# Kernel tuning notes

Hardware: AMD Instinct MI355X
Metric: run time of the kernel (lower is better)

The kernel has to match this reference:

```python
import jax, jax.numpy as jnp
import numpy as np

D = 1024          # d_input_feature
GCN_OUTS = [1024, 512, 256]
DEC_OUTS = [512, 1024, 1024]  # reversed[1:] + [d_input_feature]
EPS = 1e-3        # keras LayerNormalization default epsilon


def _ln(x, gamma, beta):
    m = jnp.mean(x, axis=-1, keepdims=True)
    v = jnp.mean(jnp.square(x - m), axis=-1, keepdims=True)
    return gamma * (x - m) * jax.lax.rsqrt(v + EPS) + beta


def _gcn(x, A, W, b, act):
    # message passing with dense adjacency: act((A @ x) @ W + b)
    h = jnp.einsum('bij,bjd->bid', A, x)
    return act(h @ W + b)


def setup_inputs() -> dict:
    key = jax.random.key(0)
    ks = jax.random.split(key, 40)
    B, DG, DC, NTT = 16384, 772, 100, 128
    inp = {
        't_1': jax.random.randint(ks[0], (B,), 0, NTT),
        'g_1': jax.random.normal(ks[1], (B, DG), jnp.float32),
        'c_1': jax.random.normal(ks[2], (B, DC), jnp.float32),
        'A_1': jax.random.uniform(ks[3], (B, 3, 3), jnp.float32),
        't_2': jax.random.randint(ks[4], (B,), 0, NTT),
        'g_2': jax.random.normal(ks[5], (B, DG), jnp.float32),
        'c_2': jax.random.normal(ks[6], (B, DC), jnp.float32),
        'A_2': jax.random.uniform(ks[7], (B, 3, 3), jnp.float32),
        'embed': jax.random.normal(ks[8], (NTT, D), jnp.float32) * 0.02,
        'Wt': jax.random.normal(ks[9], (D, D), jnp.float32) / np.sqrt(D),
        'bt': jnp.zeros((D,), jnp.float32),
        'Wg': jax.random.normal(ks[10], (DG, D), jnp.float32) / np.sqrt(DG),
        'bg': jnp.zeros((D,), jnp.float32),
        'Wc': jax.random.normal(ks[11], (DC, D), jnp.float32) / np.sqrt(DC),
        'bc': jnp.zeros((D,), jnp.float32),
        'ln_t_g': jnp.ones((D,), jnp.float32), 'ln_t_b': jnp.zeros((D,), jnp.float32),
        'ln_g_g': jnp.ones((D,), jnp.float32), 'ln_g_b': jnp.zeros((D,), jnp.float32),
        'ln_c_g': jnp.ones((D,), jnp.float32), 'ln_c_b': jnp.zeros((D,), jnp.float32),
    }
    d_in = D
    for i, d_out in enumerate(GCN_OUTS):
        inp[f'enc_W{i}'] = jax.random.normal(ks[12 + i], (d_in, d_out), jnp.float32) / np.sqrt(d_in)
        inp[f'enc_b{i}'] = jnp.zeros((d_out,), jnp.float32)
        d_in = d_out
    for i, d_out in enumerate(DEC_OUTS):
        inp[f'dec_W{i}'] = jax.random.normal(ks[20 + i], (d_in, d_out), jnp.float32) / np.sqrt(d_in)
        inp[f'dec_b{i}'] = jnp.zeros((d_out,), jnp.float32)
        d_in = d_out
    return inp


def _branch(t, g, c, embed, Wt, bt, Wg, bg, Wc, bc,
            ln_t_g, ln_t_b, ln_g_g, ln_g_b, ln_c_g, ln_c_b):
    te = embed[t]                               # [B, D]
    te = jax.nn.relu(te @ Wt + bt)
    ge = jax.nn.relu(g @ Wg + bg)
    ce = jax.nn.relu(c @ Wc + bc)
    te = _ln(te, ln_t_g, ln_t_b)
    ge = _ln(ge, ln_g_g, ln_g_b)
    ce = _ln(ce, ln_c_g, ln_c_b)
    return jnp.stack([te, ge, ce], axis=1)      # [B, 3, D]


def _encoder(X, A, enc):
    x = X
    for W, b in enc:
        x = _gcn(x, A, W, b, jax.nn.relu)
    return x


def _decoder(Z, A, dec):
    x = Z
    for W, b in dec:
        x = _gcn(x, A, W, b, jax.nn.silu)       # swish
    return x


def reference(t_1, g_1, c_1, A_1, t_2, g_2, c_2, A_2,
              embed, Wt, bt, Wg, bg, Wc, bc,
              ln_t_g, ln_t_b, ln_g_g, ln_g_b, ln_c_g, ln_c_b,
              enc_W0, enc_b0, enc_W1, enc_b1, enc_W2, enc_b2,
              dec_W0, dec_b0, dec_W1, dec_b1, dec_W2, dec_b2):
    enc = [(enc_W0, enc_b0), (enc_W1, enc_b1), (enc_W2, enc_b2)]
    dec = [(dec_W0, dec_b0), (dec_W1, dec_b1), (dec_W2, dec_b2)]
    bargs = (embed, Wt, bt, Wg, bg, Wc, bc,
             ln_t_g, ln_t_b, ln_g_g, ln_g_b, ln_c_g, ln_c_b)

    X_1 = _branch(t_1, g_1, c_1, *bargs)
    X_2 = _branch(t_2, g_2, c_2, *bargs)
    Z_1 = _encoder(X_1, A_1, enc)
    Z_2 = _encoder(X_2, A_2, enc)
    Z_loss = jnp.square(Z_1 - Z_2)              # [B, 3, 256]

    # GAE reconstruction path (recomputes X per the original code)
    X_h_1 = _decoder(Z_1, A_1, dec)
    X_h_2 = _decoder(Z_2, A_2, dec)
    X_loss = (jnp.square(X_1 - X_h_1) + jnp.square(X_2 - X_h_2)) / 2.0  # [B, 3, D]
    return Z_loss, X_loss
```

## Files before the change

### kernel.cpp

```cpp
#include <hip/hip_runtime.h>


typedef __attribute__((ext_vector_type(8))) short s16x8;
typedef __attribute__((ext_vector_type(4))) short s16x4;
typedef __attribute__((ext_vector_type(4))) float f32x4;

#define DEV static __device__ __forceinline__

DEV float b2f(ushort u) { return __builtin_bit_cast(float, (unsigned)u << 16); }
DEV ushort f2b(float f) {
  unsigned x = __builtin_bit_cast(unsigned, f);
  unsigned r = x + 0x7fffu + ((x >> 16) & 1u);
  return (ushort)(r >> 16);
}

typedef const __attribute__((address_space(1))) void* gas_ptr;
typedef __attribute__((address_space(3))) void* las_ptr;

template<int ACT>
__global__ __launch_bounds__(512, 2) void gemm256(
    const ushort* __restrict__ A, const ushort* __restrict__ BT,
    const float* __restrict__ bias, ushort* __restrict__ C,
    int M, int N, int K)
{
  __shared__ __align__(16) ushort ldsbuf[65536];
  char* Lb = (char*)ldsbuf;

  const int tid = threadIdx.x, lane = tid & 63, w = tid >> 6;
  const int wm = w >> 2, wn = w & 3;

  const int gx  = gridDim.x;
  const int nwg = gx * gridDim.y;
  const int wid = blockIdx.y * gx + blockIdx.x;
  const int q   = nwg >> 3;
  const int Lw  = (wid & 7) * q + (wid >> 3);
  const int bn  = Lw % gx;
  const int bm  = Lw / gx;

  const ushort* Abase = A  + (size_t)bm * 256 * K;
  const ushort* Bbase = BT + (size_t)bn * 256 * K;
  const int T = K >> 6;

  const int srow = w * 8 + (lane >> 3);
  const int scol = (((lane & 7) ^ (lane >> 3)) << 3);

#define STAGE(buf, m, half, Gb, k0)                                          \
  {                                                                          \
    _Pragma("unroll") for (int j = 0; j < 2; ++j) {                          \
      const ushort* _src = (Gb) + (size_t)((half)*128 + j*64 + srow) * K     \
                           + (k0) + scol;                                    \
      ushort* _dst = (ushort*)(Lb + ((buf)*2 + (m)) * 32768                  \
                               + ((half)*128 + j*64 + w*8) * 128);           \
      __builtin_amdgcn_global_load_lds((gas_ptr)_src, (las_ptr)_dst, 16,0,0);\
    }                                                                        \
  }

  const int lr = lane & 15, lk = lane >> 4;

  f32x4 acc[8][4];
  #pragma unroll
  for (int i = 0; i < 8; ++i)
    #pragma unroll
    for (int j = 0; j < 4; ++j) acc[i][j] = f32x4{0.f, 0.f, 0.f, 0.f};

#define PHASE(c, mh, nh, STG, VM)                                            \
  {                                                                          \
    s16x8 af[4][2], bf[2][2];                                                \
    _Pragma("unroll") for (int i = 0; i < 4; ++i)                            \
      _Pragma("unroll") for (int kk = 0; kk < 2; ++kk) {                     \
        const int r = (mh)*128 + wm*64 + i*16 + lr;                          \
        const int cb = kk*64 + lk*16;                                        \
        af[i][kk] = *(const s16x8*)(Lb + ((c)*2 + 0)*32768 + r*128           \
                                    + (cb ^ ((r & 7) << 4)));                \
      }                                                                      \
    _Pragma("unroll") for (int p = 0; p < 2; ++p)                            \
      _Pragma("unroll") for (int kk = 0; kk < 2; ++kk) {                     \
        const int r = (nh)*128 + wn*32 + p*16 + lr;                          \
        const int cb = kk*64 + lk*16;                                        \
        bf[p][kk] = *(const s16x8*)(Lb + ((c)*2 + 1)*32768 + r*128           \
                                    + (cb ^ ((r & 7) << 4)));                \
      }                                                                      \
    STG;                                                                     \
    __builtin_amdgcn_s_barrier();                                            \
    asm volatile("s_waitcnt lgkmcnt(0)" ::: "memory");                       \
    __builtin_amdgcn_sched_barrier(0);                                       \
    __builtin_amdgcn_s_setprio(1);                                           \
    _Pragma("unroll") for (int i = 0; i < 4; ++i)                            \
      _Pragma("unroll") for (int p = 0; p < 2; ++p)                          \
        _Pragma("unroll") for (int kk = 0; kk < 2; ++kk)                     \
          acc[(mh)*4 + i][(nh)*2 + p] =                                      \
              __builtin_amdgcn_mfma_f32_16x16x32_bf16(                       \
                  af[i][kk], bf[p][kk], acc[(mh)*4 + i][(nh)*2 + p], 0,0,0); \
    __builtin_amdgcn_s_setprio(0);                                           \
    VM;                                                                      \
    __builtin_amdgcn_s_barrier();                                            \
  }

#define VM4 asm volatile("s_waitcnt vmcnt(4)" ::: "memory")

  STAGE(0, 0, 0, Abase, 0);
  STAGE(0, 1, 0, Bbase, 0);
  STAGE(0, 0, 1, Abase, 0);
  STAGE(0, 1, 1, Bbase, 0);
  STAGE(1, 0, 0, Abase, 64);
  STAGE(1, 1, 0, Bbase, 64);
  asm volatile("s_waitcnt vmcnt(4)" ::: "memory");
  __builtin_amdgcn_s_barrier();

  for (int t = 0; t < T; t += 2) {
    const int k1 = (t + 1) * 64;
    const int k2 = ((t + 2 < T) ? (t + 2) : (t + 2 - T)) * 64;
    const int k3 = ((t + 3 < T) ? (t + 3) : (t + 3 - T)) * 64;
    PHASE(0, 0, 0, STAGE(1, 0, 1, Abase, k1), );
    PHASE(0, 0, 1, STAGE(1, 1, 1, Bbase, k1), );
    PHASE(0, 1, 0, STAGE(0, 0, 0, Abase, k2), );
    PHASE(0, 1, 1, STAGE(0, 1, 0, Bbase, k2), VM4);
    PHASE(1, 0, 0, STAGE(0, 0, 1, Abase, k2), );
    PHASE(1, 0, 1, STAGE(0, 1, 1, Bbase, k2), );
    PHASE(1, 1, 0, STAGE(1, 0, 0, Abase, k3), );
    PHASE(1, 1, 1, STAGE(1, 1, 0, Bbase, k3), VM4);
  }

  const int row0 = bm * 256, col0 = bn * 256;
  #pragma unroll
  for (int mi = 0; mi < 8; ++mi) {
    const int row = row0 + (mi >> 2) * 128 + wm * 64 + (mi & 3) * 16 + lk * 4;
    #pragma unroll
    for (int ni = 0; ni < 4; ++ni) {
      const int col = col0 + (ni >> 1) * 128 + wn * 32 + (ni & 1) * 16 + lr;
      const float bv = bias[col];
      #pragma unroll
      for (int r = 0; r < 4; ++r) {
        float v = acc[mi][ni][r] + bv;
        if (ACT == 0) v = fmaxf(v, 0.f);
        else          v = v / (1.f + __expf(-v));
        C[(size_t)(row + r) * N + col] = f2b(v);
      }
    }
  }
#undef PHASE
#undef STAGE
#undef VM4
}

template<int ACT>
__global__ __launch_bounds__(256) void gemm_bt(
    const ushort* __restrict__ A, const ushort* __restrict__ BT,
    const float* __restrict__ bias, ushort* __restrict__ C,
    int M, int N, int K)
{
  __shared__ ushort As[128 * 64];
  __shared__ ushort Bs[128 * 64];

  const int tid  = threadIdx.x;
  const int lane = tid & 63;
  const int w    = tid >> 6;

  const int gx  = gridDim.x;
  const int nwg = gx * gridDim.y;
  const int wid = blockIdx.y * gx + blockIdx.x;
  const int q   = nwg >> 3;
  const int L   = (wid & 7) * q + (wid >> 3);
  const int bn  = L % gx;
  const int bm  = L / gx;

  const int wm = w >> 1, wn = w & 1;
  const int lr = lane & 15;
  const int lk = lane >> 4;

  const ushort* Abase = A  + (size_t)bm * 128 * K;
  const ushort* Bbase = BT + (size_t)bn * 128 * K;
  const int srow = w * 8 + (lane >> 3);
  const int scol = (lane & 7) * 8;

  f32x4 acc[4][4];
  #pragma unroll
  for (int i = 0; i < 4; i++)
    #pragma unroll
    for (int j = 0; j < 4; j++) acc[i][j] = f32x4{0.f, 0.f, 0.f, 0.f};

  for (int k0 = 0; k0 < K; k0 += 64) {
    #pragma unroll
    for (int i = 0; i < 4; i++) {
      const int r = srow + i * 32;
      __builtin_amdgcn_global_load_lds(
          (gas_ptr)(Abase + (size_t)r * K + k0 + scol),
          (las_ptr)(As + w * 512 + i * 2048), 16, 0, 0);
    }
    #pragma unroll
    for (int i = 0; i < 4; i++) {
      const int r = srow + i * 32;
      __builtin_amdgcn_global_load_lds(
          (gas_ptr)(Bbase + (size_t)r * K + k0 + scol),
          (las_ptr)(Bs + w * 512 + i * 2048), 16, 0, 0);
    }
    __syncthreads();

    #pragma unroll
    for (int kc = 0; kc < 64; kc += 32) {
      s16x8 af[4], bf[4];
      #pragma unroll
      for (int mi = 0; mi < 4; mi++)
        af[mi] = *(const s16x8*)&As[(wm * 64 + mi * 16 + lr) * 64 + kc + lk * 8];
      #pragma unroll
      for (int ni = 0; ni < 4; ni++)
        bf[ni] = *(const s16x8*)&Bs[(wn * 64 + ni * 16 + lr) * 64 + kc + lk * 8];
      #pragma unroll
      for (int mi = 0; mi < 4; mi++)
        #pragma unroll
        for (int ni = 0; ni < 4; ni++)
          acc[mi][ni] = __builtin_amdgcn_mfma_f32_16x16x32_bf16(
              af[mi], bf[ni], acc[mi][ni], 0, 0, 0);
    }
    __syncthreads();
  }

  const int row0 = bm * 128 + wm * 64;
  const int col0 = bn * 128 + wn * 64;
  #pragma unroll
  for (int ni = 0; ni < 4; ni++) {
    const int col = col0 + ni * 16 + lr;
    const float bv = bias[col];
    #pragma unroll
    for (int mi = 0; mi < 4; mi++) {
      const int row = row0 + mi * 16 + lk * 4;
      #pragma unroll
      for (int r = 0; r < 4; r++) {
        float v = acc[mi][ni][r] + bv;
        if (ACT == 0) v = fmaxf(v, 0.f);
        else          v = v / (1.f + __expf(-v));
        C[(size_t)(row + r) * N + col] = f2b(v);
      }
    }
  }
}

__global__ void trans_conv(const float* __restrict__ W, ushort* __restrict__ WT,
                           int K, int N, int Kpad)
{
  __shared__ float tile[32][33];
  const int n0 = blockIdx.x * 32, k0 = blockIdx.y * 32;
  const int tx = threadIdx.x, ty = threadIdx.y;
  #pragma unroll
  for (int r = 0; r < 4; r++) {
    const int k = k0 + ty + r * 8;
    tile[ty + r * 8][tx] = (k < K) ? W[(size_t)k * N + n0 + tx] : 0.f;
  }
  __syncthreads();
  #pragma unroll
  for (int r = 0; r < 4; r++) {
    const int n = n0 + ty + r * 8;
    WT[(size_t)n * Kpad + k0 + tx] = f2b(tile[tx][ty + r * 8]);
  }
}

__global__ void conv_pad(const float* __restrict__ in, ushort* __restrict__ out,
                         int R, int Cin, int Cpad)
{
  const int gid = blockIdx.x * 256 + threadIdx.x;
  if (gid >= R * Cpad) return;
  const int r = gid / Cpad, c = gid - r * Cpad;
  out[gid] = (c < Cin) ? f2b(in[(size_t)r * Cin + c]) : (ushort)0;
}

DEV void ln_row(const ushort* __restrict__ in, const float* __restrict__ gamma,
                const float* __restrict__ beta, ushort* __restrict__ outp,
                int tid, float* red)
{
  s16x4 v = *(const s16x4*)&in[tid * 4];
  const float x0 = b2f((ushort)v[0]), x1 = b2f((ushort)v[1]);
  const float x2 = b2f((ushort)v[2]), x3 = b2f((ushort)v[3]);
  float s = x0 + x1 + x2 + x3;
  float qq = x0 * x0 + x1 * x1 + x2 * x2 + x3 * x3;
  #pragma unroll
  for (int o = 32; o > 0; o >>= 1) { s += __shfl_down(s, o); qq += __shfl_down(qq, o); }
  const int wv = tid >> 6, lane = tid & 63;
  __syncthreads();
  if (lane == 0) { red[wv] = s; red[4 + wv] = qq; }
  __syncthreads();
  s  = red[0] + red[1] + red[2] + red[3];
  qq = red[4] + red[5] + red[6] + red[7];
  const float m   = s * (1.f / 1024.f);
  const float var = qq * (1.f / 1024.f) - m * m;
  const float rs  = rsqrtf(var + 1e-3f);
  const int c = tid * 4;
  s16x4 o;
  o[0] = (short)f2b(gamma[c + 0] * ((x0 - m) * rs) + beta[c + 0]);
  o[1] = (short)f2b(gamma[c + 1] * ((x1 - m) * rs) + beta[c + 1]);
  o[2] = (short)f2b(gamma[c + 2] * ((x2 - m) * rs) + beta[c + 2]);
  o[3] = (short)f2b(gamma[c + 3] * ((x3 - m) * rs) + beta[c + 3]);
  *(s16x4*)&outp[c] = o;
}

__global__ void ln_te(const ushort* __restrict__ in, const float* __restrict__ g,
                      const float* __restrict__ b, ushort* __restrict__ out)
{
  __shared__ float red[8];
  ln_row(in + (size_t)blockIdx.x * 1024, g, b,
         out + (size_t)blockIdx.x * 1024, threadIdx.x, red);
}

__global__ void assembleX(const int* __restrict__ t, const ushort* __restrict__ tetab,
                          const ushort* __restrict__ ge, const ushort* __restrict__ ce,
                          const float* __restrict__ gG, const float* __restrict__ gB,
                          const float* __restrict__ cG, const float* __restrict__ cB,
                          ushort* __restrict__ X)
{
  __shared__ float red[8];
  const int b = blockIdx.x, tid = threadIdx.x;
  const int tt = t[b];
  *(s16x4*)&X[(size_t)b * 3072 + tid * 4] =
      *(const s16x4*)&tetab[(size_t)tt * 1024 + tid * 4];
  ln_row(ge + (size_t)b * 1024, gG, gB, X + (size_t)b * 3072 + 1024, tid, red);
  ln_row(ce + (size_t)b * 1024, cG, cB, X + (size_t)b * 3072 + 2048, tid, red);
}

__global__ void mix3(const ushort* __restrict__ x, const float* __restrict__ Am,
                     ushort* __restrict__ out, int d, int lg, int nB)
{
  const int gid = blockIdx.x * 256 + threadIdx.x;
  const int b = gid >> lg;
  if (b >= nB) return;
  const int c8 = (gid & ((1 << lg) - 1)) << 3;
  const ushort* xb = x   + (size_t)b * 3 * d + c8;
  ushort*       ob = out + (size_t)b * 3 * d + c8;
  s16x8 x0 = *(const s16x8*)xb;
  s16x8 x1 = *(const s16x8*)(xb + d);
  s16x8 x2 = *(const s16x8*)(xb + 2 * d);
  float f0[8], f1[8], f2[8];
  #pragma unroll
  for (int e = 0; e < 8; e++) {
    f0[e] = b2f((ushort)x0[e]); f1[e] = b2f((ushort)x1[e]); f2[e] = b2f((ushort)x2[e]);
  }
  const float* Ab = Am + (size_t)b * 9;
  #pragma unroll
  for (int j = 0; j < 3; j++) {
    const float a0 = Ab[j * 3], a1 = Ab[j * 3 + 1], a2 = Ab[j * 3 + 2];
    s16x8 o;
    #pragma unroll
    for (int e = 0; e < 8; e++)
      o[e] = (short)f2b(a0 * f0[e] + a1 * f1[e] + a2 * f2[e]);
    *(s16x8*)(ob + j * d) = o;
  }
}

__global__ void zloss_k(const ushort* __restrict__ z1, const ushort* __restrict__ z2,
                        float* __restrict__ out, int n8)
{
  const int gid = blockIdx.x * 256 + threadIdx.x;
  if (gid >= n8) return;
  const size_t i = (size_t)gid * 8;
  s16x8 a = *(const s16x8*)&z1[i];
  s16x8 b = *(const s16x8*)&z2[i];
  f32x4 o0, o1;
  #pragma unroll
  for (int e = 0; e < 4; e++) {
    float d0 = b2f((ushort)a[e]) - b2f((ushort)b[e]);
    float d1 = b2f((ushort)a[e + 4]) - b2f((ushort)b[e + 4]);
    o0[e] = d0 * d0; o1[e] = d1 * d1;
  }
  *(f32x4*)&out[i] = o0; *(f32x4*)&out[i + 4] = o1;
}

template<int ADD>
__global__ void xloss_k(const ushort* __restrict__ X, const ushort* __restrict__ Xh,
                        float* __restrict__ out, int n8)
{
  const int gid = blockIdx.x * 256 + threadIdx.x;
  if (gid >= n8) return;
  const size_t i = (size_t)gid * 8;
  s16x8 a = *(const s16x8*)&X[i];
  s16x8 b = *(const s16x8*)&Xh[i];
  f32x4 o0, o1;
  #pragma unroll
  for (int e = 0; e < 4; e++) {
    float d0 = b2f((ushort)a[e]) - b2f((ushort)b[e]);
    float d1 = b2f((ushort)a[e + 4]) - b2f((ushort)b[e + 4]);
    o0[e] = 0.5f * d0 * d0; o1[e] = 0.5f * d1 * d1;
  }
  if (ADD) {
    f32x4 p0 = *(const f32x4*)&out[i];
    f32x4 p1 = *(const f32x4*)&out[i + 4];
    #pragma unroll
    for (int e = 0; e < 4; e++) { o0[e] += p0[e]; o1[e] += p1[e]; }
  }
  *(f32x4*)&out[i] = o0; *(f32x4*)&out[i + 4] = o1;
}

extern "C" void kernel_launch(void* const* d_in, const int* in_sizes, int n_in,
                              void* d_out, int out_size, void* d_ws, size_t ws_size,
                              hipStream_t stream)
{
  const int B = 16384, S = 3 * B;
  const int*   t1 = (const int*)d_in[0];
  const float* g1 = (const float*)d_in[1];
  const float* c1 = (const float*)d_in[2];
  const float* A1 = (const float*)d_in[3];
  const int*   t2 = (const int*)d_in[4];
  const float* g2 = (const float*)d_in[5];
  const float* c2 = (const float*)d_in[6];
  const float* A2 = (const float*)d_in[7];
  const float* embed = (const float*)d_in[8];
  const float* Wt = (const float*)d_in[9];  const float* bt = (const float*)d_in[10];
  const float* Wg = (const float*)d_in[11]; const float* bg = (const float*)d_in[12];
  const float* Wc = (const float*)d_in[13]; const float* bc = (const float*)d_in[14];
  const float* lntg = (const float*)d_in[15]; const float* lntb = (const float*)d_in[16];
  const float* lngg = (const float*)d_in[17]; const float* lngb = (const float*)d_in[18];
  const float* lncg = (const float*)d_in[19]; const float* lncb = (const float*)d_in[20];
  const float* eW0 = (const float*)d_in[21]; const float* eb0 = (const float*)d_in[22];
  const float* eW1 = (const float*)d_in[23]; const float* eb1 = (const float*)d_in[24];
  const float* eW2 = (const float*)d_in[25]; const float* eb2 = (const float*)d_in[26];
  const float* dW0 = (const float*)d_in[27]; const float* db0 = (const float*)d_in[28];
  const float* dW1 = (const float*)d_in[29]; const float* db1 = (const float*)d_in[30];
  const float* dW2 = (const float*)d_in[31]; const float* db2 = (const float*)d_in[32];
  float* out = (float*)d_out;
  (void)in_sizes; (void)n_in; (void)out_size; (void)ws_size;

  char* ws = (char*)d_ws; size_t off = 0;
  auto alloc = [&](size_t bytes) -> void* {
    void* p = ws + off; off += (bytes + 255) & ~(size_t)255; return p;
  };
  ushort* WtT  = (ushort*)alloc((size_t)1024 * 1024 * 2);
  ushort* WgT  = (ushort*)alloc((size_t)1024 * 896 * 2);
  ushort* WcT  = (ushort*)alloc((size_t)1024 * 128 * 2);
  ushort* E0T  = (ushort*)alloc((size_t)1024 * 1024 * 2);
  ushort* E1T  = (ushort*)alloc((size_t)512 * 1024 * 2);
  ushort* E2T  = (ushort*)alloc((size_t)256 * 512 * 2);
  ushort* D0T  = (ushort*)alloc((size_t)512 * 256 * 2);
  ushort* D1T  = (ushort*)alloc((size_t)1024 * 512 * 2);
  ushort* D2T  = (ushort*)alloc((size_t)1024 * 1024 * 2);
  ushort* embB = (ushort*)alloc((size_t)128 * 1024 * 2);
  ushort* teraw= (ushort*)alloc((size_t)128 * 1024 * 2);
  ushort* tetab= (ushort*)alloc((size_t)128 * 1024 * 2);
  ushort* gB[2] = {(ushort*)alloc((size_t)B * 896 * 2), (ushort*)alloc((size_t)B * 896 * 2)};
  ushort* cB[2] = {(ushort*)alloc((size_t)B * 128 * 2), (ushort*)alloc((size_t)B * 128 * 2)};
  ushort* zB[2] = {(ushort*)alloc((size_t)S * 256 * 2), (ushort*)alloc((size_t)S * 256 * 2)};
  ushort* Xb = (ushort*)alloc((size_t)S * 1024 * 2);
  ushort* b0 = (ushort*)alloc((size_t)S * 1024 * 2);
  ushort* b1 = (ushort*)alloc((size_t)S * 1024 * 2);

  const dim3 TB(32, 8);
  trans_conv<<<dim3(32, 32), TB, 0, stream>>>(Wt,  WtT, 1024, 1024, 1024);
  trans_conv<<<dim3(32, 28), TB, 0, stream>>>(Wg,  WgT,  772, 1024,  896);
  trans_conv<<<dim3(32,  4), TB, 0, stream>>>(Wc,  WcT,  100, 1024,  128);
  trans_conv<<<dim3(32, 32), TB, 0, stream>>>(eW0, E0T, 1024, 1024, 1024);
  trans_conv<<<dim3(16, 32), TB, 0, stream>>>(eW1, E1T, 1024,  512, 1024);
  trans_conv<<<dim3( 8, 16), TB, 0, stream>>>(eW2, E2T,  512,  256,  512);
  trans_conv<<<dim3(16,  8), TB, 0, stream>>>(dW0, D0T,  256,  512,  256);
  trans_conv<<<dim3(32, 16), TB, 0, stream>>>(dW1, D1T,  512, 1024,  512);
  trans_conv<<<dim3(32, 32), TB, 0, stream>>>(dW2, D2T, 1024, 1024, 1024);
  conv_pad<<<512, 256, 0, stream>>>(embed, embB, 128, 1024, 1024);
  conv_pad<<<(B * 896 + 255) / 256, 256, 0, stream>>>(g1, gB[0], B, 772, 896);
  conv_pad<<<(B * 896 + 255) / 256, 256, 0, stream>>>(g2, gB[1], B, 772, 896);
  conv_pad<<<B * 128 / 256, 256, 0, stream>>>(c1, cB[0], B, 100, 128);
  conv_pad<<<B * 128 / 256, 256, 0, stream>>>(c2, cB[1], B, 100, 128);
  gemm_bt<0><<<dim3(8, 1), 256, 0, stream>>>(embB, WtT, bt, teraw, 128, 1024, 1024);
  ln_te<<<128, 256, 0, stream>>>(teraw, lntg, lntb, tetab);

  const size_t ZLEN = (size_t)S * 256;
  for (int br = 0; br < 2; ++br) {
    const int*   t    = br ? t2 : t1;
    const float* Aadj = br ? A2 : A1;
    gemm256<0><<<dim3(4, B / 256), 512, 0, stream>>>(gB[br], WgT, bg, b0, B, 1024, 896);
    gemm256<0><<<dim3(4, B / 256), 512, 0, stream>>>(cB[br], WcT, bc, b1, B, 1024, 128);
    assembleX<<<B, 256, 0, stream>>>(t, tetab, b0, b1, lngg, lngb, lncg, lncb, Xb);
    mix3<<<(B << 7) / 256, 256, 0, stream>>>(Xb, Aadj, b0, 1024, 7, B);
    gemm256<0><<<dim3(4, S / 256), 512, 0, stream>>>(b0, E0T, eb0, b1, S, 1024, 1024);
    mix3<<<(B << 7) / 256, 256, 0, stream>>>(b1, Aadj, b0, 1024, 7, B);
    gemm256<0><<<dim3(2, S / 256), 512, 0, stream>>>(b0, E1T, eb1, b1, S, 512, 1024);
    mix3<<<(B << 6) / 256, 256, 0, stream>>>(b1, Aadj, b0, 512, 6, B);
    gemm256<0><<<dim3(1, S / 256), 512, 0, stream>>>(b0, E2T, eb2, zB[br], S, 256, 512);
    mix3<<<(B << 5) / 256, 256, 0, stream>>>(zB[br], Aadj, b0, 256, 5, B);
    gemm256<1><<<dim3(2, S / 256), 512, 0, stream>>>(b0, D0T, db0, b1, S, 512, 256);
    mix3<<<(B << 6) / 256, 256, 0, stream>>>(b1, Aadj, b0, 512, 6, B);
    gemm256<1><<<dim3(4, S / 256), 512, 0, stream>>>(b0, D1T, db1, b1, S, 1024, 512);
    mix3<<<(B << 7) / 256, 256, 0, stream>>>(b1, Aadj, b0, 1024, 7, B);
    gemm256<1><<<dim3(4, S / 256), 512, 0, stream>>>(b0, D2T, db2, b1, S, 1024, 1024);
    if (br == 0)
      xloss_k<0><<<S * 1024 / 8 / 256, 256, 0, stream>>>(Xb, b1, out + ZLEN, S * 1024 / 8);
    else
      xloss_k<1><<<S * 1024 / 8 / 256, 256, 0, stream>>>(Xb, b1, out + ZLEN, S * 1024 / 8);
  }
  zloss_k<<<S * 256 / 8 / 256, 256, 0, stream>>>(zB[0], zB[1], out, S * 256 / 8);
}
```

Measured before the change: 1.627 ms.

## Fuse loss computations into GEMM epilogues and halve pipeline phases per k-step

Moves the Z and X reconstruction losses into the epilogues of the final encoder and decoder GEMMs, removing the separate loss kernels and the bf16 round-trip of the decoder output. The GEMM main loop is also restructured so each phase computes both N halves and issues two stage loads, halving barrier count with adjusted vmcnt waits. This raises register pressure for B fragments and changes the prefetch distance.

```diff
diff --git a/kernel.cpp b/kernel.cpp
--- a/kernel.cpp
+++ b/kernel.cpp
@@ -17,11 +17,12 @@
 typedef const __attribute__((address_space(1))) void* gas_ptr;
 typedef __attribute__((address_space(3))) void* las_ptr;
 
-template<int ACT>
+template<int ACT, int LOSS>
 __global__ __launch_bounds__(512, 2) void gemm256(
     const ushort* __restrict__ A, const ushort* __restrict__ BT,
     const float* __restrict__ bias, ushort* __restrict__ C,
-    int M, int N, int K)
+    int M, int N, int K,
+    const ushort* __restrict__ Xref, float* __restrict__ lossOut, int lossAdd)
 {
   __shared__ __align__(16) ushort ldsbuf[65536];
   char* Lb = (char*)ldsbuf;
@@ -63,9 +64,9 @@
     #pragma unroll
     for (int j = 0; j < 4; ++j) acc[i][j] = f32x4{0.f, 0.f, 0.f, 0.f};
 
-#define PHASE(c, mh, nh, STG, VM)                                            \
+#define PHASE(c, mh, STG, VM)                                                \
   {                                                                          \
-    s16x8 af[4][2], bf[2][2];                                                \
+    s16x8 af[4][2], bf[2][2][2];                                             \
     _Pragma("unroll") for (int i = 0; i < 4; ++i)                            \
       _Pragma("unroll") for (int kk = 0; kk < 2; ++kk) {                     \
         const int r = (mh)*128 + wm*64 + i*16 + lr;                          \
@@ -73,52 +74,50 @@
         af[i][kk] = *(const s16x8*)(Lb + ((c)*2 + 0)*32768 + r*128           \
                                     + (cb ^ ((r & 7) << 4)));                \
       }                                                                      \
-    _Pragma("unroll") for (int p = 0; p < 2; ++p)                            \
-      _Pragma("unroll") for (int kk = 0; kk < 2; ++kk) {                     \
-        const int r = (nh)*128 + wn*32 + p*16 + lr;                          \
-        const int cb = kk*64 + lk*16;                                        \
-        bf[p][kk] = *(const s16x8*)(Lb + ((c)*2 + 1)*32768 + r*128           \
-                                    + (cb ^ ((r & 7) << 4)));                \
-      }                                                                      \
+    _Pragma("unroll") for (int nh = 0; nh < 2; ++nh)                         \
+      _Pragma("unroll") for (int p = 0; p < 2; ++p)                          \
+        _Pragma("unroll") for (int kk = 0; kk < 2; ++kk) {                   \
+          const int r = nh*128 + wn*32 + p*16 + lr;                          \
+          const int cb = kk*64 + lk*16;                                      \
+          bf[nh][p][kk] = *(const s16x8*)(Lb + ((c)*2 + 1)*32768 + r*128     \
+                                          + (cb ^ ((r & 7) << 4)));          \
+        }                                                                    \
     STG;                                                                     \
     __builtin_amdgcn_s_barrier();                                            \
     asm volatile("s_waitcnt lgkmcnt(0)" ::: "memory");                       \
     __builtin_amdgcn_sched_barrier(0);                                       \
     __builtin_amdgcn_s_setprio(1);                                           \
     _Pragma("unroll") for (int i = 0; i < 4; ++i)                            \
-      _Pragma("unroll") for (int p = 0; p < 2; ++p)                          \
-        _Pragma("unroll") for (int kk = 0; kk < 2; ++kk)                     \
-          acc[(mh)*4 + i][(nh)*2 + p] =                                      \
-              __builtin_amdgcn_mfma_f32_16x16x32_bf16(                       \
-                  af[i][kk], bf[p][kk], acc[(mh)*4 + i][(nh)*2 + p], 0,0,0); \
+      _Pragma("unroll") for (int nh = 0; nh < 2; ++nh)                       \
+        _Pragma("unroll") for (int p = 0; p < 2; ++p)                        \
+          _Pragma("unroll") for (int kk = 0; kk < 2; ++kk)                   \
+            acc[(mh)*4 + i][nh*2 + p] =                                      \
+                __builtin_amdgcn_mfma_f32_16x16x32_bf16(                     \
+                    af[i][kk], bf[nh][p][kk], acc[(mh)*4 + i][nh*2 + p],     \
+                    0, 0, 0);                                                \
     __builtin_amdgcn_s_setprio(0);                                           \
     VM;                                                                      \
     __builtin_amdgcn_s_barrier();                                            \
   }
 
-#define VM4 asm volatile("s_waitcnt vmcnt(4)" ::: "memory")
+#define VM2 asm volatile("s_waitcnt vmcnt(2)" ::: "memory")
 
   STAGE(0, 0, 0, Abase, 0);
+  STAGE(0, 0, 1, Abase, 0);
   STAGE(0, 1, 0, Bbase, 0);
-  STAGE(0, 0, 1, Abase, 0);
   STAGE(0, 1, 1, Bbase, 0);
   STAGE(1, 0, 0, Abase, 64);
-  STAGE(1, 1, 0, Bbase, 64);
-  asm volatile("s_waitcnt vmcnt(4)" ::: "memory");
+  asm volatile("s_waitcnt vmcnt(2)" ::: "memory");
   __builtin_amdgcn_s_barrier();
 
   for (int t = 0; t < T; t += 2) {
     const int k1 = (t + 1) * 64;
     const int k2 = ((t + 2 < T) ? (t + 2) : (t + 2 - T)) * 64;
     const int k3 = ((t + 3 < T) ? (t + 3) : (t + 3 - T)) * 64;
-    PHASE(0, 0, 0, STAGE(1, 0, 1, Abase, k1), );
-    PHASE(0, 0, 1, STAGE(1, 1, 1, Bbase, k1), );
-    PHASE(0, 1, 0, STAGE(0, 0, 0, Abase, k2), );
-    PHASE(0, 1, 1, STAGE(0, 1, 0, Bbase, k2), VM4);
-    PHASE(1, 0, 0, STAGE(0, 0, 1, Abase, k2), );
-    PHASE(1, 0, 1, STAGE(0, 1, 1, Bbase, k2), );
-    PHASE(1, 1, 0, STAGE(1, 0, 0, Abase, k3), );
-    PHASE(1, 1, 1, STAGE(1, 1, 0, Bbase, k3), VM4);
+    PHASE(0, 0, STAGE(1, 0, 1, Abase, k1); STAGE(1, 1, 0, Bbase, k1), );
+    PHASE(0, 1, STAGE(1, 1, 1, Bbase, k1); STAGE(0, 0, 0, Abase, k2), VM2);
+    PHASE(1, 0, STAGE(0, 0, 1, Abase, k2); STAGE(0, 1, 0, Bbase, k2), );
+    PHASE(1, 1, STAGE(0, 1, 1, Bbase, k2); STAGE(1, 0, 0, Abase, k3), VM2);
   }
 
   const int row0 = bm * 256, col0 = bn * 256;
@@ -134,13 +133,25 @@
         float v = acc[mi][ni][r] + bv;
         if (ACT == 0) v = fmaxf(v, 0.f);
         else          v = v / (1.f + __expf(-v));
-        C[(size_t)(row + r) * N + col] = f2b(v);
+        const size_t idx = (size_t)(row + r) * N + col;
+        if (LOSS == 0) {
+          C[idx] = f2b(v);
+        } else if (LOSS == 1) {
+          const float d = b2f(Xref[idx]) - v;
+          float l = 0.5f * d * d;
+          if (lossAdd) l += lossOut[idx];
+          lossOut[idx] = l;
+        } else {
+          C[idx] = f2b(v);
+          const float d = b2f(Xref[idx]) - v;
+          lossOut[idx] = d * d;
+        }
       }
     }
   }
 #undef PHASE
 #undef STAGE
-#undef VM4
+#undef VM2
 }
 
 template<int ACT>
@@ -342,49 +353,6 @@
       o[e] = (short)f2b(a0 * f0[e] + a1 * f1[e] + a2 * f2[e]);
     *(s16x8*)(ob + j * d) = o;
   }
-}
-
-__global__ void zloss_k(const ushort* __restrict__ z1, const ushort* __restrict__ z2,
-                        float* __restrict__ out, int n8)
-{
-  const int gid = blockIdx.x * 256 + threadIdx.x;
-  if (gid >= n8) return;
-  const size_t i = (size_t)gid * 8;
-  s16x8 a = *(const s16x8*)&z1[i];
-  s16x8 b = *(const s16x8*)&z2[i];
-  f32x4 o0, o1;
-  #pragma unroll
-  for (int e = 0; e < 4; e++) {
-    float d0 = b2f((ushort)a[e]) - b2f((ushort)b[e]);
-    float d1 = b2f((ushort)a[e + 4]) - b2f((ushort)b[e + 4]);
-    o0[e] = d0 * d0; o1[e] = d1 * d1;
-  }
-  *(f32x4*)&out[i] = o0; *(f32x4*)&out[i + 4] = o1;
-}
-
-template<int ADD>
-__global__ void xloss_k(const ushort* __restrict__ X, const ushort* __restrict__ Xh,
-                        float* __restrict__ out, int n8)
-{
-  const int gid = blockIdx.x * 256 + threadIdx.x;
-  if (gid >= n8) return;
-  const size_t i = (size_t)gid * 8;
-  s16x8 a = *(const s16x8*)&X[i];
-  s16x8 b = *(const s16x8*)&Xh[i];
-  f32x4 o0, o1;
-  #pragma unroll
-  for (int e = 0; e < 4; e++) {
-    float d0 = b2f((ushort)a[e]) - b2f((ushort)b[e]);
-    float d1 = b2f((ushort)a[e + 4]) - b2f((ushort)b[e + 4]);
-    o0[e] = 0.5f * d0 * d0; o1[e] = 0.5f * d1 * d1;
-  }
-  if (ADD) {
-    f32x4 p0 = *(const f32x4*)&out[i];
-    f32x4 p1 = *(const f32x4*)&out[i + 4];
-    #pragma unroll
-    for (int e = 0; e < 4; e++) { o0[e] += p0[e]; o1[e] += p1[e]; }
-  }
-  *(f32x4*)&out[i] = o0; *(f32x4*)&out[i + 4] = o1;
 }
 
 extern "C" void kernel_launch(void* const* d_in, const int* in_sizes, int n_in,
@@ -461,25 +429,23 @@
   for (int br = 0; br < 2; ++br) {
     const int*   t    = br ? t2 : t1;
     const float* Aadj = br ? A2 : A1;
-    gemm256<0><<<dim3(4, B / 256), 512, 0, stream>>>(gB[br], WgT, bg, b0, B, 1024, 896);
-    gemm256<0><<<dim3(4, B / 256), 512, 0, stream>>>(cB[br], WcT, bc, b1, B, 1024, 128);
+    gemm256<0,0><<<dim3(4, B / 256), 512, 0, stream>>>(gB[br], WgT, bg, b0, B, 1024, 896, nullptr, nullptr, 0);
+    gemm256<0,0><<<dim3(4, B / 256), 512, 0, stream>>>(cB[br], WcT, bc, b1, B, 1024, 128, nullptr, nullptr, 0);
     assembleX<<<B, 256, 0, stream>>>(t, tetab, b0, b1, lngg, lngb, lncg, lncb, Xb);
     mix3<<<(B << 7) / 256, 256, 0, stream>>>(Xb, Aadj, b0, 1024, 7, B);
-    gemm256<0><<<dim3(4, S / 256), 512, 0, stream>>>(b0, E0T, eb0, b1, S, 1024, 1024);
+    gemm256<0,0><<<dim3(4, S / 256), 512, 0, stream>>>(b0, E0T, eb0, b1, S, 1024, 1024, nullptr, nullptr, 0);
     mix3<<<(B << 7) / 256, 256, 0, stream>>>(b1, Aadj, b0, 1024, 7, B);
-    gemm256<0><<<dim3(2, S / 256), 512, 0, stream>>>(b0, E1T, eb1, b1, S, 512, 1024);
+    gemm256<0,0><<<dim3(2, S / 256), 512, 0, stream>>>(b0, E1T, eb1, b1, S, 512, 1024, nullptr, nullptr, 0);
     mix3<<<(B << 6) / 256, 256, 0, stream>>>(b1, Aadj, b0, 512, 6, B);
-    gemm256<0><<<dim3(1, S / 256), 512, 0, stream>>>(b0, E2T, eb2, zB[br], S, 256, 512);
+    if (br == 0)
+      gemm256<0,0><<<dim3(1, S / 256), 512, 0, stream>>>(b0, E2T, eb2, zB[0], S, 256, 512, nullptr, nullptr, 0);
+    else
+      gemm256<0,2><<<dim3(1, S / 256), 512, 0, stream>>>(b0, E2T, eb2, zB[1], S, 256, 512, zB[0], out, 0);
     mix3<<<(B << 5) / 256, 256, 0, stream>>>(zB[br], Aadj, b0, 256, 5, B);
-    gemm256<1><<<dim3(2, S / 256), 512, 0, stream>>>(b0, D0T, db0, b1, S, 512, 256);
+    gemm256<1,0><<<dim3(2, S / 256), 512, 0, stream>>>(b0, D0T, db0, b1, S, 512, 256, nullptr, nullptr, 0);
     mix3<<<(B << 6) / 256, 256, 0, stream>>>(b1, Aadj, b0, 512, 6, B);
-    gemm256<1><<<dim3(4, S / 256), 512, 0, stream>>>(b0, D1T, db1, b1, S, 1024, 512);
+    gemm256<1,0><<<dim3(4, S / 256), 512, 0, stream>>>(b0, D1T, db1, b1, S, 1024, 512, nullptr, nullptr, 0);
     mix3<<<(B << 7) / 256, 256, 0, stream>>>(b1, Aadj, b0, 1024, 7, B);
-    gemm256<1><<<dim3(4, S / 256), 512, 0, stream>>>(b0, D2T, db2, b1, S, 1024, 1024);
-    if (br == 0)
-      xloss_k<0><<<S * 1024 / 8 / 256, 256, 0, stream>>>(Xb, b1, out + ZLEN, S * 1024 / 8);
-    else
-      xloss_k<1><<<S * 1024 / 8 / 256, 256, 0, stream>>>(Xb, b1, out + ZLEN, S * 1024 / 8);
-  }
-  zloss_k<<<S * 256 / 8 / 256, 256, 0, stream>>>(zB[0], zB[1], out, S * 256 / 8);
-}
+    gemm256<1,1><<<dim3(4, S / 256), 512, 0, stream>>>(b0, D2T, db2, b1, S, 1024, 1024, Xb, out + ZLEN, br);
+  }
+}
```

Measured after the change: 1.913 ms. 1.18x slower.

## Reorder GEMM K-loop phases to reuse LDS fragments and deepen prefetch

Applied to the files above, without the earlier changes.

Restructures the 256x256 bf16 GEMM main loop from eight phases per two K-tiles into four phases per K-tile ordered (0,0),(0,1),(1,1),(1,0). Consecutive phases share A or B fragments, so fewer LDS reads are issued per tile. The staging schedule changes so that prefetch of the next tiles overlaps the MFMA work, with vmcnt(6) waits. This adds tricky buffer-reuse hazards, since stages write into the current buffer while its other halves are still being read.

```diff
diff --git a/kernel.cpp b/kernel.cpp
--- a/kernel.cpp
+++ b/kernel.cpp
@@ -46,79 +46,88 @@
 
 #define STAGE(buf, m, half, Gb, k0)                                          \
   {                                                                          \
-    _Pragma("unroll") for (int j = 0; j < 2; ++j) {                          \
-      const ushort* _src = (Gb) + (size_t)((half)*128 + j*64 + srow) * K     \
+    _Pragma("unroll") for (int _j = 0; _j < 2; ++_j) {                       \
+      const ushort* _src = (Gb) + (size_t)((half)*128 + _j*64 + srow) * K    \
                            + (k0) + scol;                                    \
       ushort* _dst = (ushort*)(Lb + ((buf)*2 + (m)) * 32768                  \
-                               + ((half)*128 + j*64 + w*8) * 128);           \
+                               + ((half)*128 + _j*64 + w*8) * 128);          \
       __builtin_amdgcn_global_load_lds((gas_ptr)_src, (las_ptr)_dst, 16,0,0);\
     }                                                                        \
   }
 
   const int lr = lane & 15, lk = lane >> 4;
 
+#define READ_A(dst, c, mh)                                                   \
+  _Pragma("unroll") for (int _i = 0; _i < 4; ++_i)                           \
+    _Pragma("unroll") for (int _kk = 0; _kk < 2; ++_kk) {                    \
+      const int _r   = (mh)*128 + wm*64 + _i*16 + lr;                        \
+      const int _cbb = _kk*64 + lk*16;                                       \
+      dst[_i][_kk] = *(const s16x8*)(Lb + ((c)*2 + 0)*32768 + _r*128         \
+                                     + (_cbb ^ ((_r & 7) << 4)));            \
+    }
+#define READ_B(dst, c, nh)                                                   \
+  _Pragma("unroll") for (int _p = 0; _p < 2; ++_p)                           \
+    _Pragma("unroll") for (int _kk = 0; _kk < 2; ++_kk) {                    \
+      const int _r   = (nh)*128 + wn*32 + _p*16 + lr;                        \
+      const int _cbb = _kk*64 + lk*16;                                       \
+      dst[_p][_kk] = *(const s16x8*)(Lb + ((c)*2 + 1)*32768 + _r*128         \
+                                     + (_cbb ^ ((_r & 7) << 4)));            \
+    }
+
+#define MFMA_Q(mh, nh)                                                       \
+  _Pragma("unroll") for (int _i = 0; _i < 4; ++_i)                           \
+    _Pragma("unroll") for (int _p = 0; _p < 2; ++_p)                         \
+      _Pragma("unroll") for (int _kk = 0; _kk < 2; ++_kk)                    \
+        acc[(mh)*4 + _i][(nh)*2 + _p] =                                      \
+            __builtin_amdgcn_mfma_f32_16x16x32_bf16(                         \
+                af[_i][_kk], bf[_p][_kk], acc[(mh)*4 + _i][(nh)*2 + _p],     \
+                0, 0, 0);
+
+#define MIDBAR  do { __builtin_amdgcn_s_barrier();                           \
+                     asm volatile("s_waitcnt lgkmcnt(0)" ::: "memory");      \
+                     __builtin_amdgcn_sched_barrier(0);                      \
+                     __builtin_amdgcn_s_setprio(1); } while (0)
+#define ENDBAR  do { __builtin_amdgcn_s_setprio(0);                          \
+                     __builtin_amdgcn_s_barrier(); } while (0)
+
   f32x4 acc[8][4];
   #pragma unroll
   for (int i = 0; i < 8; ++i)
     #pragma unroll
     for (int j = 0; j < 4; ++j) acc[i][j] = f32x4{0.f, 0.f, 0.f, 0.f};
-
-#define PHASE(c, mh, nh, STG, VM)                                            \
-  {                                                                          \
-    s16x8 af[4][2], bf[2][2];                                                \
-    _Pragma("unroll") for (int i = 0; i < 4; ++i)                            \
-      _Pragma("unroll") for (int kk = 0; kk < 2; ++kk) {                     \
-        const int r = (mh)*128 + wm*64 + i*16 + lr;                          \
-        const int cb = kk*64 + lk*16;                                        \
-        af[i][kk] = *(const s16x8*)(Lb + ((c)*2 + 0)*32768 + r*128           \
-                                    + (cb ^ ((r & 7) << 4)));                \
-      }                                                                      \
-    _Pragma("unroll") for (int p = 0; p < 2; ++p)                            \
-      _Pragma("unroll") for (int kk = 0; kk < 2; ++kk) {                     \
-        const int r = (nh)*128 + wn*32 + p*16 + lr;                          \
-        const int cb = kk*64 + lk*16;                                        \
-        bf[p][kk] = *(const s16x8*)(Lb + ((c)*2 + 1)*32768 + r*128           \
-                                    + (cb ^ ((r & 7) << 4)));                \
-      }                                                                      \
-    STG;                                                                     \
-    __builtin_amdgcn_s_barrier();                                            \
-    asm volatile("s_waitcnt lgkmcnt(0)" ::: "memory");                       \
-    __builtin_amdgcn_sched_barrier(0);                                       \
-    __builtin_amdgcn_s_setprio(1);                                           \
-    _Pragma("unroll") for (int i = 0; i < 4; ++i)                            \
-      _Pragma("unroll") for (int p = 0; p < 2; ++p)                          \
-        _Pragma("unroll") for (int kk = 0; kk < 2; ++kk)                     \
-          acc[(mh)*4 + i][(nh)*2 + p] =                                      \
-              __builtin_amdgcn_mfma_f32_16x16x32_bf16(                       \
-                  af[i][kk], bf[p][kk], acc[(mh)*4 + i][(nh)*2 + p], 0,0,0); \
-    __builtin_amdgcn_s_setprio(0);                                           \
-    VM;                                                                      \
-    __builtin_amdgcn_s_barrier();                                            \
-  }
-
-#define VM4 asm volatile("s_waitcnt vmcnt(4)" ::: "memory")
 
   STAGE(0, 0, 0, Abase, 0);
   STAGE(0, 1, 0, Bbase, 0);
+  STAGE(0, 1, 1, Bbase, 0);
   STAGE(0, 0, 1, Abase, 0);
-  STAGE(0, 1, 1, Bbase, 0);
   STAGE(1, 0, 0, Abase, 64);
-  STAGE(1, 1, 0, Bbase, 64);
-  asm volatile("s_waitcnt vmcnt(4)" ::: "memory");
+  STAGE(1, 1, 1, Bbase, 64);
+  STAGE(1, 0, 1, Abase, 64);
+  asm volatile("s_waitcnt vmcnt(6)" ::: "memory");
   __builtin_amdgcn_s_barrier();
 
-  for (int t = 0; t < T; t += 2) {
-    const int k1 = (t + 1) * 64;
-    const int k2 = ((t + 2 < T) ? (t + 2) : (t + 2 - T)) * 64;
-    const int k3 = ((t + 3 < T) ? (t + 3) : (t + 3 - T)) * 64;
-    PHASE(0, 0, 0, STAGE(1, 0, 1, Abase, k1), );
-    PHASE(0, 0, 1, STAGE(1, 1, 1, Bbase, k1), );
-    PHASE(0, 1, 0, STAGE(0, 0, 0, Abase, k2), );
-    PHASE(0, 1, 1, STAGE(0, 1, 0, Bbase, k2), VM4);
-    PHASE(1, 0, 0, STAGE(0, 0, 1, Abase, k2), );
-    PHASE(1, 0, 1, STAGE(0, 1, 1, Bbase, k2), );
-    PHASE(1, 1, 0, STAGE(1, 0, 0, Abase, k3), );
-    PHASE(1, 1, 1, STAGE(1, 1, 0, Bbase, k3), VM4);
+  for (int t = 0; t < T; ++t) {
+    const int cbuf = t & 1, nbuf = cbuf ^ 1;
+    const int k1 = ((t + 1 < T) ? t + 1 : t + 1 - T) * 64;
+    const int k2 = ((t + 2 < T) ? t + 2 : t + 2 - T) * 64;
+    s16x8 af[4][2], bf[2][2];
+    READ_A(af, cbuf, 0);
+    READ_B(bf, cbuf, 0);
+    STAGE(nbuf, 1, 0, Bbase, k1);
+    asm volatile("s_waitcnt lgkmcnt(8)" ::: "memory");
+    MIDBAR; MFMA_Q(0, 0); ENDBAR;
+    READ_B(bf, cbuf, 1);
+    STAGE(cbuf, 0, 0, Abase, k2);
+    MIDBAR; MFMA_Q(0, 1); ENDBAR;
+    READ_A(af, cbuf, 1);
+    STAGE(cbuf, 1, 1, Bbase, k2);
+    MIDBAR; MFMA_Q(1, 1); ENDBAR;
+    READ_B(bf, cbuf, 0);
+    STAGE(cbuf, 0, 1, Abase, k2);
+    MIDBAR; MFMA_Q(1, 0);
+    __builtin_amdgcn_s_setprio(0);
+    asm volatile("s_waitcnt vmcnt(6)" ::: "memory");
+    __builtin_amdgcn_s_barrier();
   }
 
   const int row0 = bm * 256, col0 = bn * 256;
@@ -138,9 +147,12 @@
       }
     }
   }
-#undef PHASE
 #undef STAGE
-#undef VM4
+#undef READ_A
+#undef READ_B
+#undef MFMA_Q
+#undef MIDBAR
+#undef ENDBAR
 }
 
 template<int ACT>
```

Measured after the change: 1.572 ms. 1.03x faster.
